# Kernel optimization log

Measured on AMD Instinct MI355X. Metric: run time of the kernel, lower is better.

Reference implementation:

```python
import jax, jax.numpy as jnp
import numpy as np
import math

N = 100000      # n_entities
C = 128         # channel
E = 600000      # n_edges
NNZ = 1000000   # interact_mat nnz
NU = 50000      # n_users
NREL = 25       # n_relations
H = 4           # n_heads
DK = C // H     # d_k


def setup_inputs() -> dict:
    key = jax.random.key(0)
    ks = jax.random.split(key, 13)
    s = 1.0 / math.sqrt(C)
    return {
        "entity_emb": jax.random.normal(ks[0], (N, C), jnp.float32),
        "W_Q": jax.random.normal(ks[1], (C, C), jnp.float32) * s,
        "W_K": jax.random.normal(ks[2], (C, C), jnp.float32) * s,
        "W_V": jax.random.normal(ks[3], (C, C), jnp.float32) * s,
        "W_O": jax.random.normal(ks[4], (C, C), jnp.float32) * s,
        "relation_att": jax.random.normal(ks[5], (NREL - 1, H, DK, DK), jnp.float32) * s,
        "relation_msg": jax.random.normal(ks[6], (NREL - 1, H, DK, DK), jnp.float32) * s,
        "relation_emb": jax.random.normal(ks[7], (NREL - 1, C), jnp.float32),
        "edge_index": jax.random.randint(ks[8], (2, E), 0, N, jnp.int32),
        "edge_type": jax.random.randint(ks[9], (E,), 1, NREL, jnp.int32),
        "im_rows": jax.random.randint(ks[10], (NNZ,), 0, NU, jnp.int32),
        "im_cols": jax.random.randint(ks[11], (NNZ,), 0, N, jnp.int32),
        "im_vals": jax.random.uniform(ks[12], (NNZ,), jnp.float32),
        "n_users": NU,
    }


def reference(entity_emb, W_Q, W_K, W_V, W_O, relation_att, relation_msg,
              relation_emb, edge_index, edge_type, im_rows, im_cols, im_vals,
              n_users):
    n_entities, channel = entity_emb.shape
    n_heads, d_k = H, channel // H
    head, tail = edge_index[0], edge_index[1]
    rel = edge_type - 1

    # Step 1: heterogeneous mutual attention
    q = (entity_emb[head] @ W_Q).reshape(-1, n_heads, d_k)            # [E,H,Dk]
    k = (entity_emb[tail] @ W_K).reshape(-1, n_heads, d_k)
    k = jnp.einsum("ehd,ehdk->ehk", k, relation_att[rel])
    score = (q * k).sum(-1) / math.sqrt(d_k)                           # [E,H]

    # Step 2: heterogeneous message passing
    v = (entity_emb[tail] @ W_V).reshape(-1, n_heads, d_k)
    v = jnp.einsum("ehd,ehdk->ehk", v, relation_msg[rel])

    # scatter_softmax over target node id (head)
    seg_max = jax.ops.segment_max(score, head, num_segments=n_entities)  # [N,H]
    ex = jnp.exp(score - seg_max[head])
    denom = jax.ops.segment_sum(ex, head, num_segments=n_entities)
    attn = ex / denom[head]                                              # [E,H]

    agg = (v * attn[..., None]).reshape(-1, n_heads * d_k) @ W_O         # [E,C]
    entity_agg = jax.ops.segment_sum(agg, head, num_segments=n_entities)

    # user aggregate: sparse [NU,N] @ entity_emb
    user_agg = jax.ops.segment_sum(entity_emb[im_cols] * im_vals[:, None],
                                   im_rows, num_segments=n_users)
    return entity_agg, user_agg
```

## Files before the change

### kernel.cpp

```cpp
#include <hip/hip_runtime.h>
#include <hip/hip_bf16.h>
#include <math.h>

typedef __attribute__((ext_vector_type(8))) unsigned short u16x8;
typedef __attribute__((ext_vector_type(4))) unsigned short u16x4;
typedef __attribute__((ext_vector_type(8))) short bf16x8;
typedef __attribute__((ext_vector_type(4))) float f32x4;

#define NRELMAX 32

__device__ __forceinline__ float b2f(unsigned short u) {
    return __uint_as_float(((unsigned)u) << 16);
}
__device__ __forceinline__ unsigned short f2b(float v) {
    __hip_bfloat16 b = __float2bfloat16(v);
    return *reinterpret_cast<unsigned short*>(&b);
}

__device__ __forceinline__ bf16x8 lda_frag(const __hip_bfloat16* p) {
    return *(const bf16x8*)p;
}
__device__ __forceinline__ void st_o(__hip_bfloat16* p, float v) { *p = __float2bfloat16(v); }
__device__ __forceinline__ void st_o(float* p, float v) { *p = v; }

template <typename TO>
__device__ __forceinline__ void gemm_body(const __hip_bfloat16* __restrict__ A,
                                          const __hip_bfloat16* __restrict__ Wt,
                                          TO* __restrict__ out, int n, int blk)
{
    const int tid = threadIdx.x;
    const int w = tid >> 6;
    const int l = tid & 63;
    const int q = l >> 4;
    const int c16 = l & 15;
    const int wr = (w >> 1) * 64;
    const int wc = (w & 1) * 64;
    const long row0 = (long)blk * 128;

    f32x4 acc[4][4] = {};
    #pragma unroll
    for (int ks = 0; ks < 4; ++ks) {
        bf16x8 af[4];
        #pragma unroll
        for (int rb = 0; rb < 4; ++rb) {
            long r = row0 + wr + rb * 16 + c16;
            if (r >= n) r = n - 1;
            af[rb] = lda_frag(A + r * 128 + ks * 32 + q * 8);
        }
        #pragma unroll
        for (int cb = 0; cb < 4; ++cb) {
            bf16x8 wf = *(const bf16x8*)(Wt + (size_t)(wc + cb * 16 + c16) * 128 + ks * 32 + q * 8);
            #pragma unroll
            for (int rb = 0; rb < 4; ++rb)
                acc[rb][cb] = __builtin_amdgcn_mfma_f32_16x16x32_bf16(af[rb], wf, acc[rb][cb], 0, 0, 0);
        }
    }
    #pragma unroll
    for (int rb = 0; rb < 4; ++rb) {
        #pragma unroll
        for (int r = 0; r < 4; ++r) {
            long row = row0 + wr + rb * 16 + q * 4 + r;
            if (row < n) {
                #pragma unroll
                for (int cb = 0; cb < 4; ++cb)
                    st_o(out + row * 128 + wc + cb * 16 + c16, acc[rb][cb][r]);
            }
        }
    }
}

template <typename TO>
__global__ __launch_bounds__(256) void mfma_gemm(const __hip_bfloat16* __restrict__ A,
                                                 const __hip_bfloat16* __restrict__ Wt,
                                                 TO* __restrict__ out, int n)
{
    gemm_body<TO>(A, Wt, out, n, blockIdx.x);
}

__global__ __launch_bounds__(256) void qkv3(const __hip_bfloat16* __restrict__ A,
                                            const __hip_bfloat16* __restrict__ WtQ,
                                            const __hip_bfloat16* __restrict__ WtK,
                                            const __hip_bfloat16* __restrict__ WtV,
                                            __hip_bfloat16* __restrict__ Qb,
                                            __hip_bfloat16* __restrict__ Kb,
                                            __hip_bfloat16* __restrict__ Vb, int n, int gg)
{
    int which = blockIdx.x / gg;
    int blk = blockIdx.x % gg;
    const __hip_bfloat16* Wt = (which == 0) ? WtQ : (which == 1) ? WtK : WtV;
    __hip_bfloat16* Out = (which == 0) ? Qb : (which == 1) ? Kb : Vb;
    gemm_body<__hip_bfloat16>(A, Wt, Out, n, blk);
}

__global__ __launch_bounds__(256) void prep_count(
    const float* __restrict__ W0, const float* __restrict__ W1,
    const float* __restrict__ W2, const float* __restrict__ W3,
    __hip_bfloat16* __restrict__ T0, __hip_bfloat16* __restrict__ T1,
    __hip_bfloat16* __restrict__ T2, __hip_bfloat16* __restrict__ T3,
    const float* __restrict__ att, const float* __restrict__ msg,
    __hip_bfloat16* __restrict__ Atab, __hip_bfloat16* __restrict__ Mtab, int nrel,
    const float* __restrict__ emb, __hip_bfloat16* __restrict__ embb, long n4,
    const int* __restrict__ head, const int* __restrict__ etyp,
    const int* __restrict__ irow,
    unsigned* __restrict__ ecnt, unsigned* __restrict__ ucnt,
    unsigned* __restrict__ rcnt, int* __restrict__ plocalE,
    int* __restrict__ plocalU, int E, int NNZ,
    int nbW, int nbT, int nbC)
{
    __shared__ unsigned lcnt[NRELMAX];
    const int tid = threadIdx.x;
    const int bx = blockIdx.x;
    if (bx < nbW) {
        int t = bx * 256 + tid;
        int w = t >> 14, r = t & 16383;
        const float* W = (w == 0) ? W0 : (w == 1) ? W1 : (w == 2) ? W2 : W3;
        __hip_bfloat16* T = (w == 0) ? T0 : (w == 1) ? T1 : (w == 2) ? T2 : T3;
        int k = r >> 7, c = r & 127;
        T[(size_t)c * 128 + k] = __float2bfloat16(W[(size_t)k * 128 + c]);
        return;
    }
    if (bx < nbW + nbT) {
        int t = (bx - nbW) * 256 + tid;
        int tot = nrel * 4096;
        if (t >= 2 * tot) return;
        const float* src = (t < tot) ? att : msg;
        __hip_bfloat16* dst = (t < tot) ? Atab : Mtab;
        int u = (t < tot) ? t : t - tot;
        int rel = u >> 12, rem = u & 4095;
        int h = rem >> 10;  rem &= 1023;
        int s2 = rem >> 9;  rem &= 511;
        int lane = rem >> 3, j = rem & 7;
        int g = lane >> 4, c = lane & 15;
        dst[u] = __float2bfloat16(src[(size_t)rel * 4096 + h * 1024 + s2 * 16 + (g * 8 + j) * 32 + c]);
        return;
    }
    if (bx < nbW + nbT + nbC) {
        long i = ((long)(bx - nbW - nbT) * 256 + tid) * 4;
        if (i >= n4 * 4) return;
        float4 v = *(const float4*)(emb + i);
        u16x4 o;
        o[0] = f2b(v.x); o[1] = f2b(v.y); o[2] = f2b(v.z); o[3] = f2b(v.w);
        *(u16x4*)(embb + i) = o;
        return;
    }
    if (tid < NRELMAX) lcnt[tid] = 0;
    __syncthreads();
    int i = (bx - nbW - nbT - nbC) * 256 + tid;
    if (i < E) {
        unsigned p = atomicAdd(&ecnt[head[i]], 1u);
        plocalE[i] = (int)p;
        atomicAdd(&lcnt[etyp[i] - 1], 1u);
    }
    if (i < NNZ) {
        unsigned p = atomicAdd(&ucnt[irow[i]], 1u);
        plocalU[i] = (int)p;
    }
    __syncthreads();
    if (tid < NRELMAX) {
        unsigned c = lcnt[tid];
        if (c) atomicAdd(&rcnt[tid], c);
    }
}

__global__ __launch_bounds__(1024) void scan_p1(
    unsigned* __restrict__ ecnt, int n_e, unsigned* __restrict__ bsumE,
    unsigned* __restrict__ ucnt, int n_u, unsigned* __restrict__ bsumU, int nbE)
{
    unsigned* buf; unsigned* bsum; int n; int blk;
    if ((int)blockIdx.x < nbE) { buf = ecnt; bsum = bsumE; n = n_e; blk = blockIdx.x; }
    else { buf = ucnt; bsum = bsumU; n = n_u; blk = blockIdx.x - nbE; }
    __shared__ unsigned sh[1024];
    int i = blk * 1024 + threadIdx.x;
    unsigned v = (i < n) ? buf[i] : 0u;
    sh[threadIdx.x] = v;
    __syncthreads();
    for (int off = 1; off < 1024; off <<= 1) {
        unsigned t = (threadIdx.x >= (unsigned)off) ? sh[threadIdx.x - off] : 0u;
        __syncthreads();
        sh[threadIdx.x] += t;
        __syncthreads();
    }
    if (i < n) buf[i] = sh[threadIdx.x] - v;
    if (threadIdx.x == 1023) bsum[blk] = sh[1023];
}

__global__ __launch_bounds__(1024) void scan_p2(
    unsigned* __restrict__ bsumE, int nbE, unsigned* __restrict__ bsumU, int nbU,
    const unsigned* __restrict__ rcnt, unsigned* __restrict__ rcur,
    unsigned* __restrict__ rend, unsigned* __restrict__ rnext, int nrel)
{
    if (blockIdx.x == 2) {
        if (threadIdx.x == 0) {
            unsigned acc = 0;
            for (int r = 0; r < nrel; ++r) {
                rcur[r] = acc;
                rend[r] = acc + rcnt[r];
                acc += (rcnt[r] + 15u) & ~15u;
                rnext[r] = acc;
            }
        }
        return;
    }
    unsigned* bsum = (blockIdx.x == 0) ? bsumE : bsumU;
    int nb = (blockIdx.x == 0) ? nbE : nbU;
    __shared__ unsigned sh[1024];
    unsigned v = (threadIdx.x < (unsigned)nb) ? bsum[threadIdx.x] : 0u;
    sh[threadIdx.x] = v;
    __syncthreads();
    for (int off = 1; off < 1024; off <<= 1) {
        unsigned t = (threadIdx.x >= (unsigned)off) ? sh[threadIdx.x - off] : 0u;
        __syncthreads();
        sh[threadIdx.x] += t;
        __syncthreads();
    }
    if (threadIdx.x < (unsigned)nb) bsum[threadIdx.x] = sh[threadIdx.x] - v;
}

__global__ __launch_bounds__(1024) void scan_p3(
    unsigned* __restrict__ ecnt, int n_e, const unsigned* __restrict__ bsumE,
    unsigned* __restrict__ ucnt, int n_u, const unsigned* __restrict__ bsumU, int nbE)
{
    unsigned* buf; const unsigned* bsum; int n; int blk;
    if ((int)blockIdx.x < nbE) { buf = ecnt; bsum = bsumE; n = n_e; blk = blockIdx.x; }
    else { buf = ucnt; bsum = bsumU; n = n_u; blk = blockIdx.x - nbE; }
    int i = blk * 1024 + threadIdx.x;
    if (i < n) buf[i] += bsum[blk];
}

__global__ __launch_bounds__(256) void fills(
    const int* __restrict__ irow, const int* __restrict__ icol,
    const float* __restrict__ ival, const unsigned* __restrict__ ustart,
    const int* __restrict__ plocalU, int2* __restrict__ upair, int NNZ,
    const int* __restrict__ head, const int* __restrict__ tail,
    const int* __restrict__ etyp, const unsigned* __restrict__ estart,
    const int* __restrict__ plocalE, unsigned* __restrict__ rcur,
    int4* __restrict__ emeta, int E,
    const unsigned* __restrict__ rend, const unsigned* __restrict__ rnext,
    int nrel, long emax, int nbU, int nbE)
{
    __shared__ unsigned lcnt[NRELMAX];
    __shared__ unsigned lbase[NRELMAX];
    const int tid = threadIdx.x;
    const int bx = blockIdx.x;
    if (bx < nbU) {
        int i = bx * 256 + tid;
        if (i < NNZ) {
            unsigned slot = ustart[irow[i]] + (unsigned)plocalU[i];
            upair[slot] = make_int2(icol[i], __float_as_int(ival[i]));
        }
        return;
    }
    if (bx < nbU + nbE) {
        if (tid < NRELMAX) lcnt[tid] = 0;
        __syncthreads();
        int i = (bx - nbU) * 256 + tid;
        int r = 0;
        unsigned lpos = 0;
        if (i < E) {
            r = etyp[i] - 1;
            lpos = atomicAdd(&lcnt[r], 1u);
        }
        __syncthreads();
        if (tid < NRELMAX) {
            unsigned c = lcnt[tid];
            lbase[tid] = c ? atomicAdd(&rcur[tid], c) : 0u;
        }
        __syncthreads();
        if (i < E) {
            int hn = head[i];
            unsigned slot = estart[hn] + (unsigned)plocalE[i];
            emeta[lbase[r] + lpos] = make_int4(hn, tail[i], (int)slot, r);
        }
        return;
    }
    for (int r = 0; r < nrel; ++r) {
        unsigned s = rend[r], e2 = rnext[r];
        for (unsigned i = s + tid; i < e2; i += 256)
            emeta[i] = make_int4(0, 0, -1, r);
    }
    long ep = rnext[nrel - 1];
    for (long i = ep + tid; i < emax; i += 256)
        emeta[i] = make_int4(0, 0, -1, nrel - 1);
}

template <int ROUND>
__global__ __launch_bounds__(256, 2) void edge_pass(
    const __hip_bfloat16* __restrict__ Qb, const __hip_bfloat16* __restrict__ Kb,
    const __hip_bfloat16* __restrict__ Vb,
    const __hip_bfloat16* __restrict__ Atab, const __hip_bfloat16* __restrict__ Mtab,
    const int4* __restrict__ emeta, float* __restrict__ SC,
    __hip_bfloat16* __restrict__ VPh, long Epad, int chunk)
{
    const int wv = (blockIdx.x * 256 + threadIdx.x) >> 6;
    const int l = threadIdx.x & 63;
    const int g = l >> 4;
    const int c = l & 15;
    long j0 = (long)wv * chunk;
    if (j0 >= Epad) return;
    long j1 = j0 + chunk; if (j1 > Epad) j1 = Epad;

    bf16x8 aK[2][2], aM[2][2];
    int currel = -1;
    for (long pos = j0; pos < j1; pos += 16) {
        const int4 md = emeta[pos + c];
        const int rel0 = __shfl(md.w, 0, 64);
        if (rel0 != currel) {
            currel = rel0;
            #pragma unroll
            for (int hl = 0; hl < 2; ++hl) {
                const int h = ROUND * 2 + hl;
                #pragma unroll
                for (int s2 = 0; s2 < 2; ++s2) {
                    size_t idx = ((((size_t)rel0 * 4 + h) * 2 + s2) * 64 + l) * 8;
                    aK[hl][s2] = *(const bf16x8*)(Atab + idx);
                    aM[hl][s2] = *(const bf16x8*)(Mtab + idx);
                }
            }
        }
        const int tn = md.y, hn = md.x, slot = md.z;
        #pragma unroll
        for (int hl = 0; hl < 2; ++hl) {
            const int h = ROUND * 2 + hl;
            bf16x8 bk = *(const bf16x8*)(Kb + (size_t)tn * 128 + h * 32 + g * 8);
            bf16x8 bv = *(const bf16x8*)(Vb + (size_t)tn * 128 + h * 32 + g * 8);
            f32x4 z = {0.f, 0.f, 0.f, 0.f};
            f32x4 klo = __builtin_amdgcn_mfma_f32_16x16x32_bf16(aK[hl][0], bk, z, 0, 0, 0);
            f32x4 khi = __builtin_amdgcn_mfma_f32_16x16x32_bf16(aK[hl][1], bk, z, 0, 0, 0);
            f32x4 vlo = __builtin_amdgcn_mfma_f32_16x16x32_bf16(aM[hl][0], bv, z, 0, 0, 0);
            f32x4 vhi = __builtin_amdgcn_mfma_f32_16x16x32_bf16(aM[hl][1], bv, z, 0, 0, 0);
            const __hip_bfloat16* qp = Qb + (size_t)hn * 128 + h * 32;
            u16x4 q1 = *(const u16x4*)(qp + g * 4);
            u16x4 q2 = *(const u16x4*)(qp + 16 + g * 4);
            float p = 0.f;
            #pragma unroll
            for (int r = 0; r < 4; ++r)
                p += b2f(q1[r]) * klo[r] + b2f(q2[r]) * khi[r];
            p += __shfl_xor(p, 16, 64);
            p += __shfl_xor(p, 32, 64);
            if (slot >= 0) {
                if (g == 0) SC[(size_t)slot * 4 + h] = p * 0.17677669529663687f;
                u16x4 plo, phi;
                #pragma unroll
                for (int r = 0; r < 4; ++r) { plo[r] = f2b(vlo[r]); phi[r] = f2b(vhi[r]); }
                __hip_bfloat16* dst = VPh + (size_t)slot * 64 + hl * 32;
                *(u16x4*)(dst + g * 4) = plo;
                *(u16x4*)(dst + 16 + g * 4) = phi;
            }
        }
    }
}

template <int ROUND>
__global__ __launch_bounds__(256) void node_pass(
    const float* __restrict__ SC, const __hip_bfloat16* __restrict__ VPh,
    const unsigned* __restrict__ estart, __hip_bfloat16* __restrict__ M, int n, int Etot)
{
    int node = (blockIdx.x * 256 + threadIdx.x) >> 6;
    if (node >= n) return;
    int l = threadIdx.x & 63;
    int half = l >> 5;
    const int h = ROUND * 2 + half;
    unsigned beg = estart[node];
    unsigned end = (node + 1 < n) ? estart[node + 1] : (unsigned)Etot;
    float mx = -INFINITY, dn = 0.f;
    for (unsigned j = beg; j < end; ++j) {
        float s = SC[(size_t)j * 4 + h];
        float m2 = fmaxf(mx, s);
        dn = dn * __expf(mx - m2) + __expf(s - m2);
        mx = m2;
    }
    float inv = (end > beg) ? 1.f / dn : 0.f;
    float acc = 0.f;
    for (unsigned j = beg; j < end; ++j) {
        float w = __expf(SC[(size_t)j * 4 + h] - mx) * inv;
        acc = fmaf(w, __bfloat162float(VPh[(size_t)j * 64 + l]), acc);
    }
    M[(size_t)node * 128 + ROUND * 64 + l] = __float2bfloat16(acc);
}

__global__ __launch_bounds__(256) void user_gather(
    const __hip_bfloat16* __restrict__ embb, const unsigned* __restrict__ ustart,
    const int2* __restrict__ upair, float* __restrict__ out, int nu, int NNZ)
{
    int u = (blockIdx.x * 256 + threadIdx.x) >> 5;
    if (u >= nu) return;
    int l = threadIdx.x & 31;
    unsigned beg = ustart[u];
    unsigned end = (u + 1 < nu) ? ustart[u + 1] : (unsigned)NNZ;
    float a0 = 0.f, a1 = 0.f, a2 = 0.f, a3 = 0.f;
    float b0 = 0.f, b1 = 0.f, b2 = 0.f, b3 = 0.f;
    unsigned j = beg;
    for (; j + 3 < end; j += 4) {
        int2 p0 = upair[j], p1 = upair[j + 1], p2 = upair[j + 2], p3 = upair[j + 3];
        float v0 = __int_as_float(p0.y), v1 = __int_as_float(p1.y);
        float v2 = __int_as_float(p2.y), v3 = __int_as_float(p3.y);
        uint2 e0 = *(const uint2*)((const unsigned*)(embb + (size_t)p0.x * 128) + l * 2);
        uint2 e1 = *(const uint2*)((const unsigned*)(embb + (size_t)p1.x * 128) + l * 2);
        uint2 e2 = *(const uint2*)((const unsigned*)(embb + (size_t)p2.x * 128) + l * 2);
        uint2 e3 = *(const uint2*)((const unsigned*)(embb + (size_t)p3.x * 128) + l * 2);
        a0 = fmaf(b2f((unsigned short)(e0.x & 0xFFFF)), v0, a0);
        a1 = fmaf(b2f((unsigned short)(e0.x >> 16)), v0, a1);
        a2 = fmaf(b2f((unsigned short)(e0.y & 0xFFFF)), v0, a2);
        a3 = fmaf(b2f((unsigned short)(e0.y >> 16)), v0, a3);
        b0 = fmaf(b2f((unsigned short)(e1.x & 0xFFFF)), v1, b0);
        b1 = fmaf(b2f((unsigned short)(e1.x >> 16)), v1, b1);
        b2 = fmaf(b2f((unsigned short)(e1.y & 0xFFFF)), v1, b2);
        b3 = fmaf(b2f((unsigned short)(e1.y >> 16)), v1, b3);
        a0 = fmaf(b2f((unsigned short)(e2.x & 0xFFFF)), v2, a0);
        a1 = fmaf(b2f((unsigned short)(e2.x >> 16)), v2, a1);
        a2 = fmaf(b2f((unsigned short)(e2.y & 0xFFFF)), v2, a2);
        a3 = fmaf(b2f((unsigned short)(e2.y >> 16)), v2, a3);
        b0 = fmaf(b2f((unsigned short)(e3.x & 0xFFFF)), v3, b0);
        b1 = fmaf(b2f((unsigned short)(e3.x >> 16)), v3, b1);
        b2 = fmaf(b2f((unsigned short)(e3.y & 0xFFFF)), v3, b2);
        b3 = fmaf(b2f((unsigned short)(e3.y >> 16)), v3, b3);
    }
    for (; j < end; ++j) {
        int2 p0 = upair[j];
        float v0 = __int_as_float(p0.y);
        uint2 e0 = *(const uint2*)((const unsigned*)(embb + (size_t)p0.x * 128) + l * 2);
        a0 = fmaf(b2f((unsigned short)(e0.x & 0xFFFF)), v0, a0);
        a1 = fmaf(b2f((unsigned short)(e0.x >> 16)), v0, a1);
        a2 = fmaf(b2f((unsigned short)(e0.y & 0xFFFF)), v0, a2);
        a3 = fmaf(b2f((unsigned short)(e0.y >> 16)), v0, a3);
    }
    *(float4*)(out + (size_t)u * 128 + l * 4) =
        make_float4(a0 + b0, a1 + b1, a2 + b2, a3 + b3);
}

extern "C" void kernel_launch(void* const* d_in, const int* in_sizes, int n_in,
                              void* d_out, int out_size, void* d_ws, size_t ws_size,
                              hipStream_t stream)
{
    const float* emb = (const float*)d_in[0];
    const float* W_Q = (const float*)d_in[1];
    const float* W_K = (const float*)d_in[2];
    const float* W_V = (const float*)d_in[3];
    const float* W_O = (const float*)d_in[4];
    const float* att = (const float*)d_in[5];
    const float* msg = (const float*)d_in[6];
    const int* eidx  = (const int*)d_in[8];
    const int* etyp  = (const int*)d_in[9];
    const int* irow  = (const int*)d_in[10];
    const int* icol  = (const int*)d_in[11];
    const float* ival = (const float*)d_in[12];

    const int N    = in_sizes[0] / 128;
    const int E    = in_sizes[8] / 2;
    const int NNZ  = in_sizes[10];
    const int NU   = out_size / 128 - N;
    const int NREL = in_sizes[5] / 4096;

    const int* head = eidx;
    const int* tail = eidx + E;

    const int NUp = (NU + 255) & ~255;

    const size_t NC = (size_t)N * 128;
    char* p = (char*)d_ws;
    __hip_bfloat16* VPh = (__hip_bfloat16*)p; p += (size_t)E * 64 * 2;
    __hip_bfloat16* Kb  = (__hip_bfloat16*)p; p += NC * 2;
    __hip_bfloat16* Vb  = (__hip_bfloat16*)p; p += NC * 2;
    __hip_bfloat16* M   = (__hip_bfloat16*)p; p += NC * 2;
    unsigned* rcnt  = (unsigned*)p; p += 32 * 4;
    unsigned* rcur  = (unsigned*)p; p += 32 * 4;
    unsigned* rend  = (unsigned*)p; p += 32 * 4;
    unsigned* rnext = (unsigned*)p; p += 32 * 4;
    unsigned* ucnt  = (unsigned*)p; p += (size_t)NUp * 4;
    unsigned* bsumE = (unsigned*)p; p += 1024 * 4;
    unsigned* bsumU = (unsigned*)p; p += 1024 * 4;
    int2* upair     = (int2*)p;     p += (size_t)NNZ * 8;
    __hip_bfloat16* WtQ = (__hip_bfloat16*)p; p += 16384 * 2;
    __hip_bfloat16* WtK = (__hip_bfloat16*)p; p += 16384 * 2;
    __hip_bfloat16* WtV = (__hip_bfloat16*)p; p += 16384 * 2;
    __hip_bfloat16* WtO = (__hip_bfloat16*)p; p += 16384 * 2;
    __hip_bfloat16* Atab = (__hip_bfloat16*)p; p += (size_t)NREL * 4096 * 2;
    __hip_bfloat16* Mtab = (__hip_bfloat16*)p; p += (size_t)NREL * 4096 * 2;

    int* plocalU = (int*)VPh;
    int* plocalE = plocalU + NNZ;

    float* out_ent = (float*)d_out;
    float* out_usr = out_ent + NC;
    __hip_bfloat16* embb = (__hip_bfloat16*)out_ent;
    __hip_bfloat16* Qb   = (__hip_bfloat16*)((char*)d_out + NC * 2);
    const long Emax = E + 512;
    float* SC   = out_usr;
    int4* emeta = (int4*)(out_usr + (size_t)E * 4);
    unsigned* ecnt = (unsigned*)((char*)emeta + (size_t)Emax * 16);

    hipMemsetAsync(rcnt, 0, (32 * 4) * 4 + (size_t)NUp * 4, stream);
    hipMemsetAsync(ecnt, 0, (size_t)N * 4, stream);

    const int nbW = 256;
    const int nbT = (2 * NREL * 4096 + 255) / 256;
    const int nbC = (int)((NC / 4 + 255) / 256);
    const int nbX = ((NNZ > E ? NNZ : E) + 255) / 256;
    prep_count<<<nbW + nbT + nbC + nbX, 256, 0, stream>>>(
        W_Q, W_K, W_V, W_O, WtQ, WtK, WtV, WtO,
        att, msg, Atab, Mtab, NREL,
        emb, embb, (long)(NC / 4),
        head, etyp, irow, ecnt, ucnt, rcnt, plocalE, plocalU,
        E, NNZ, nbW, nbT, nbC);

    int gg = (N + 127) / 128;
    qkv3<<<3 * gg, 256, 0, stream>>>(embb, WtQ, WtK, WtV, Qb, Kb, Vb, N, gg);

    int nbE2 = (N + 1023) / 1024;
    int nbU2 = (NU + 1023) / 1024;
    scan_p1<<<nbE2 + nbU2, 1024, 0, stream>>>(ecnt, N, bsumE, ucnt, NU, bsumU, nbE2);
    scan_p2<<<3, 1024, 0, stream>>>(bsumE, nbE2, bsumU, nbU2, rcnt, rcur, rend, rnext, NREL);
    scan_p3<<<nbE2 + nbU2, 1024, 0, stream>>>(ecnt, N, bsumE, ucnt, NU, bsumU, nbE2);

    const int nbU = (NNZ + 255) / 256;
    const int nbE = (E + 255) / 256;
    fills<<<nbU + nbE + 1, 256, 0, stream>>>(
        irow, icol, ival, ucnt, plocalU, upair, NNZ,
        head, tail, etyp, ecnt, plocalE, rcur, emeta, E,
        rend, rnext, NREL, Emax, nbU, nbE);

    const int NWAVE = 16384;
    int chunk = (int)(((Emax + NWAVE - 1) / NWAVE + 15) & ~15L);
    edge_pass<0><<<NWAVE / 4, 256, 0, stream>>>(Qb, Kb, Vb, Atab, Mtab, emeta, SC, VPh, Emax, chunk);
    node_pass<0><<<(N + 3) / 4, 256, 0, stream>>>(SC, VPh, ecnt, M, N, E);
    edge_pass<1><<<NWAVE / 4, 256, 0, stream>>>(Qb, Kb, Vb, Atab, Mtab, emeta, SC, VPh, Emax, chunk);
    node_pass<1><<<(N + 3) / 4, 256, 0, stream>>>(SC, VPh, ecnt, M, N, E);

    user_gather<<<(NU + 7) / 8, 256, 0, stream>>>(embb, ucnt, upair, out_usr, NU, NNZ);

    mfma_gemm<float><<<gg, 256, 0, stream>>>(M, WtO, out_ent, N);
}
```

Baseline: 590.5 us.

## Move atomic counting into QKV GEMM launch and raise edge_pass occupancy

The atomic edge/user counting blocks move out of the prep kernel into the same launch as the Q/K/V GEMM. The latency-bound atomic work can then overlap with the compute-bound GEMM blocks instead of running alongside the conversion work. Separately, edge_pass launch bounds go from 2 to 4 blocks per CU, which pushes the compiler toward fewer registers and may cause spills. The counting blocks come first in the grid, so they are scheduled before the GEMM tiles.

Measured after the change: 583.9 us. Within noise of the previous version (-1.1%).

```diff
diff --git a/kernel.cpp b/kernel.cpp
--- a/kernel.cpp
+++ b/kernel.cpp
@@ -77,22 +77,7 @@
     gemm_body<TO>(A, Wt, out, n, blockIdx.x);
 }
 
-__global__ __launch_bounds__(256) void qkv3(const __hip_bfloat16* __restrict__ A,
-                                            const __hip_bfloat16* __restrict__ WtQ,
-                                            const __hip_bfloat16* __restrict__ WtK,
-                                            const __hip_bfloat16* __restrict__ WtV,
-                                            __hip_bfloat16* __restrict__ Qb,
-                                            __hip_bfloat16* __restrict__ Kb,
-                                            __hip_bfloat16* __restrict__ Vb, int n, int gg)
-{
-    int which = blockIdx.x / gg;
-    int blk = blockIdx.x % gg;
-    const __hip_bfloat16* Wt = (which == 0) ? WtQ : (which == 1) ? WtK : WtV;
-    __hip_bfloat16* Out = (which == 0) ? Qb : (which == 1) ? Kb : Vb;
-    gemm_body<__hip_bfloat16>(A, Wt, Out, n, blk);
-}
-
-__global__ __launch_bounds__(256) void prep_count(
+__global__ __launch_bounds__(256) void prep(
     const float* __restrict__ W0, const float* __restrict__ W1,
     const float* __restrict__ W2, const float* __restrict__ W3,
     __hip_bfloat16* __restrict__ T0, __hip_bfloat16* __restrict__ T1,
@@ -100,14 +85,8 @@
     const float* __restrict__ att, const float* __restrict__ msg,
     __hip_bfloat16* __restrict__ Atab, __hip_bfloat16* __restrict__ Mtab, int nrel,
     const float* __restrict__ emb, __hip_bfloat16* __restrict__ embb, long n4,
-    const int* __restrict__ head, const int* __restrict__ etyp,
-    const int* __restrict__ irow,
-    unsigned* __restrict__ ecnt, unsigned* __restrict__ ucnt,
-    unsigned* __restrict__ rcnt, int* __restrict__ plocalE,
-    int* __restrict__ plocalU, int E, int NNZ,
-    int nbW, int nbT, int nbC)
-{
-    __shared__ unsigned lcnt[NRELMAX];
+    int nbW, int nbT)
+{
     const int tid = threadIdx.x;
     const int bx = blockIdx.x;
     if (bx < nbW) {
@@ -134,32 +113,55 @@
         dst[u] = __float2bfloat16(src[(size_t)rel * 4096 + h * 1024 + s2 * 16 + (g * 8 + j) * 32 + c]);
         return;
     }
-    if (bx < nbW + nbT + nbC) {
-        long i = ((long)(bx - nbW - nbT) * 256 + tid) * 4;
-        if (i >= n4 * 4) return;
-        float4 v = *(const float4*)(emb + i);
-        u16x4 o;
-        o[0] = f2b(v.x); o[1] = f2b(v.y); o[2] = f2b(v.z); o[3] = f2b(v.w);
-        *(u16x4*)(embb + i) = o;
+    long i = ((long)(bx - nbW - nbT) * 256 + tid) * 4;
+    if (i >= n4 * 4) return;
+    float4 v = *(const float4*)(emb + i);
+    u16x4 o;
+    o[0] = f2b(v.x); o[1] = f2b(v.y); o[2] = f2b(v.z); o[3] = f2b(v.w);
+    *(u16x4*)(embb + i) = o;
+}
+
+__global__ __launch_bounds__(256) void qkv_count(
+    const int* __restrict__ head, const int* __restrict__ etyp,
+    const int* __restrict__ irow,
+    unsigned* __restrict__ ecnt, unsigned* __restrict__ ucnt,
+    unsigned* __restrict__ rcnt, int* __restrict__ plocalE,
+    int* __restrict__ plocalU, int E, int NNZ, int nbX,
+    const __hip_bfloat16* __restrict__ A,
+    const __hip_bfloat16* __restrict__ WtQ, const __hip_bfloat16* __restrict__ WtK,
+    const __hip_bfloat16* __restrict__ WtV,
+    __hip_bfloat16* __restrict__ Qb, __hip_bfloat16* __restrict__ Kb,
+    __hip_bfloat16* __restrict__ Vb, int n, int gg)
+{
+    __shared__ unsigned lcnt[NRELMAX];
+    const int tid = threadIdx.x;
+    const int bx = blockIdx.x;
+    if (bx < nbX) {
+        if (tid < NRELMAX) lcnt[tid] = 0;
+        __syncthreads();
+        int i = bx * 256 + tid;
+        if (i < E) {
+            unsigned p = atomicAdd(&ecnt[head[i]], 1u);
+            plocalE[i] = (int)p;
+            atomicAdd(&lcnt[etyp[i] - 1], 1u);
+        }
+        if (i < NNZ) {
+            unsigned p = atomicAdd(&ucnt[irow[i]], 1u);
+            plocalU[i] = (int)p;
+        }
+        __syncthreads();
+        if (tid < NRELMAX) {
+            unsigned c = lcnt[tid];
+            if (c) atomicAdd(&rcnt[tid], c);
+        }
         return;
     }
-    if (tid < NRELMAX) lcnt[tid] = 0;
-    __syncthreads();
-    int i = (bx - nbW - nbT - nbC) * 256 + tid;
-    if (i < E) {
-        unsigned p = atomicAdd(&ecnt[head[i]], 1u);
-        plocalE[i] = (int)p;
-        atomicAdd(&lcnt[etyp[i] - 1], 1u);
-    }
-    if (i < NNZ) {
-        unsigned p = atomicAdd(&ucnt[irow[i]], 1u);
-        plocalU[i] = (int)p;
-    }
-    __syncthreads();
-    if (tid < NRELMAX) {
-        unsigned c = lcnt[tid];
-        if (c) atomicAdd(&rcnt[tid], c);
-    }
+    int b2 = bx - nbX;
+    int which = b2 / gg;
+    int blk = b2 % gg;
+    const __hip_bfloat16* Wt = (which == 0) ? WtQ : (which == 1) ? WtK : WtV;
+    __hip_bfloat16* Out = (which == 0) ? Qb : (which == 1) ? Kb : Vb;
+    gemm_body<__hip_bfloat16>(A, Wt, Out, n, blk);
 }
 
 __global__ __launch_bounds__(1024) void scan_p1(
@@ -284,7 +286,7 @@
 }
 
 template <int ROUND>
-__global__ __launch_bounds__(256, 2) void edge_pass(
+__global__ __launch_bounds__(256, 4) void edge_pass(
     const __hip_bfloat16* __restrict__ Qb, const __hip_bfloat16* __restrict__ Kb,
     const __hip_bfloat16* __restrict__ Vb,
     const __hip_bfloat16* __restrict__ Atab, const __hip_bfloat16* __restrict__ Mtab,
@@ -495,16 +497,16 @@
     const int nbW = 256;
     const int nbT = (2 * NREL * 4096 + 255) / 256;
     const int nbC = (int)((NC / 4 + 255) / 256);
-    const int nbX = ((NNZ > E ? NNZ : E) + 255) / 256;
-    prep_count<<<nbW + nbT + nbC + nbX, 256, 0, stream>>>(
+    prep<<<nbW + nbT + nbC, 256, 0, stream>>>(
         W_Q, W_K, W_V, W_O, WtQ, WtK, WtV, WtO,
         att, msg, Atab, Mtab, NREL,
-        emb, embb, (long)(NC / 4),
-        head, etyp, irow, ecnt, ucnt, rcnt, plocalE, plocalU,
-        E, NNZ, nbW, nbT, nbC);
+        emb, embb, (long)(NC / 4), nbW, nbT);
 
     int gg = (N + 127) / 128;
-    qkv3<<<3 * gg, 256, 0, stream>>>(embb, WtQ, WtK, WtV, Qb, Kb, Vb, N, gg);
+    const int nbX = ((NNZ > E ? NNZ : E) + 255) / 256;
+    qkv_count<<<nbX + 3 * gg, 256, 0, stream>>>(
+        head, etyp, irow, ecnt, ucnt, rcnt, plocalE, plocalU, E, NNZ, nbX,
+        embb, WtQ, WtK, WtV, Qb, Kb, Vb, N, gg);
 
     int nbE2 = (N + 1023) / 1024;
     int nbU2 = (NU + 1023) / 1024;
```
